# Performance work log

Measured on AMD Instinct MI355X. Metric: run time of the kernel, lower is better.

Reference implementation:

```python
import jax, jax.numpy as jnp
import numpy as np

B = 512          # batch_size
C = 4            # num_classes
N = 16384        # grid unknowns per sample (128x128)
H = 0.0078125    # grid spacing h = 1/128


def setup_inputs() -> dict:
    key = jax.random.key(0)
    k1, k2, k3 = jax.random.split(key, 3)
    coefficients = jax.random.uniform(k1, (B, N), dtype=jnp.float32)  # positive -> A SPD
    predictions = jax.random.normal(k2, (B, C, N), dtype=jnp.float32)
    targets = jax.random.normal(k3, (B, N, C), dtype=jnp.float32)
    return {"coefficients": coefficients, "predictions": predictions, "targets": targets}


def reference(coefficients, predictions, targets):
    # A = diag(h^2 * coefficients[i]); exploit diagonality: A @ v == a * v.
    a = (H * H) * coefficients                      # [B, N] diagonal of A per sample
    preds = predictions.reshape(B, C, -1)           # predictions.view(batch_size, num_classes, -1)

    # Modified Gram-Schmidt in the A-inner product, vectorized over batch.
    ortho = []
    for j in range(C):                              # tiny fixed loop over classes
        v = preds[:, j, :]                          # [B, N]
        for e in ortho:
            proj = jnp.sum(v * (a * e), axis=-1, keepdims=True)  # <v, A e>
            v = v - proj * e
        n2 = jnp.sum(v * a * v, axis=-1, keepdims=True)          # <v, A v>
        safe = jnp.where(n2 > 0, n2, jnp.float32(1.0))
        v = jnp.where(n2 > 0, v * jax.lax.rsqrt(safe), v)        # normalize iff <v,Av> > 0
        ortho.append(v)
    Cm = jnp.stack(ortho, axis=1)                   # [B, C, N]

    # M = C_i @ A @ targets[i] for each sample -> [B, C, C]
    M = jnp.einsum('bcn,bnm->bcm', Cm * a[:, None, :], targets)
    per_sample = (jnp.float32(4.0) - jnp.sum(M * M, axis=(1, 2))) / jnp.float32(4.0)
    return jnp.mean(per_sample)
```

## Files before the change

### kernel.cpp

```cpp
#include <hip/hip_runtime.h>

#define BSZ 512
#define NC  4
#define NN  16384
#define H2  (0.0078125f * 0.0078125f)

#define BLK   512
#define SPLIT 2
#define GROUPS_PER_BLOCK (NN / 4 / SPLIT)
#define ITERS (GROUPS_PER_BLOCK / BLK)

__device__ __forceinline__ void accum_elem(float a,
                                           float p0, float p1, float p2, float p3,
                                           float tx, float ty, float tz, float tw,
                                           float* acc)
{
    float ap0 = a * p0, ap1 = a * p1, ap2 = a * p2, ap3 = a * p3;
    acc[0]  += ap0 * p0;  acc[1]  += ap0 * p1;  acc[2]  += ap0 * p2;  acc[3]  += ap0 * p3;
    acc[4]  += ap1 * p1;  acc[5]  += ap1 * p2;  acc[6]  += ap1 * p3;
    acc[7]  += ap2 * p2;  acc[8]  += ap2 * p3;
    acc[9]  += ap3 * p3;
    acc[10] += ap0 * tx;  acc[11] += ap0 * ty;  acc[12] += ap0 * tz;  acc[13] += ap0 * tw;
    acc[14] += ap1 * tx;  acc[15] += ap1 * ty;  acc[16] += ap1 * tz;  acc[17] += ap1 * tw;
    acc[18] += ap2 * tx;  acc[19] += ap2 * ty;  acc[20] += ap2 * tz;  acc[21] += ap2 * tw;
    acc[22] += ap3 * tx;  acc[23] += ap3 * ty;  acc[24] += ap3 * tz;  acc[25] += ap3 * tw;
}

__global__ __launch_bounds__(BLK)
void loss_part(const float* __restrict__ coef,
               const float* __restrict__ pred,
               const float* __restrict__ targ,
               float* __restrict__ partial)
{
    const int blk = blockIdx.x;
    const int b   = blk / SPLIT;
    const int s   = blk % SPLIT;
    const int tid = threadIdx.x;

    const float4* __restrict__ c4 = (const float4*)(coef + (size_t)b * NN);
    const float4* __restrict__ q0 = (const float4*)(pred + (size_t)b * NC * NN + 0 * NN);
    const float4* __restrict__ q1 = (const float4*)(pred + (size_t)b * NC * NN + 1 * NN);
    const float4* __restrict__ q2 = (const float4*)(pred + (size_t)b * NC * NN + 2 * NN);
    const float4* __restrict__ q3 = (const float4*)(pred + (size_t)b * NC * NN + 3 * NN);
    const float4* __restrict__ t4 = (const float4*)(targ + (size_t)b * NN * NC);

    const int g0 = s * GROUPS_PER_BLOCK;

    float acc[26];
#pragma unroll
    for (int k = 0; k < 26; ++k) acc[k] = 0.f;

    for (int k = 0; k < ITERS; ++k) {
        const int i = g0 + k * BLK + tid;
        float4 cc = c4[i];
        float4 a0 = q0[i];
        float4 a1 = q1[i];
        float4 a2 = q2[i];
        float4 a3 = q3[i];
        float4 t0 = t4[4 * i + 0];
        float4 t1 = t4[4 * i + 1];
        float4 t2 = t4[4 * i + 2];
        float4 t3 = t4[4 * i + 3];

        accum_elem(H2 * cc.x, a0.x, a1.x, a2.x, a3.x, t0.x, t0.y, t0.z, t0.w, acc);
        accum_elem(H2 * cc.y, a0.y, a1.y, a2.y, a3.y, t1.x, t1.y, t1.z, t1.w, acc);
        accum_elem(H2 * cc.z, a0.z, a1.z, a2.z, a3.z, t2.x, t2.y, t2.z, t2.w, acc);
        accum_elem(H2 * cc.w, a0.w, a1.w, a2.w, a3.w, t3.x, t3.y, t3.z, t3.w, acc);
    }

    const int lane = tid & 63;
    const int wv   = tid >> 6;
    __shared__ float red[26][8];

#pragma unroll
    for (int k = 0; k < 26; ++k) {
        float v = acc[k];
#pragma unroll
        for (int o = 32; o > 0; o >>= 1) v += __shfl_down(v, o, 64);
        if (lane == 0) red[k][wv] = v;
    }
    __syncthreads();

    if (tid < 26) {
        float v = 0.f;
#pragma unroll
        for (int w = 0; w < 8; ++w) v += red[tid][w];
        partial[(size_t)blk * 26 + tid] = v;
    }
}

__global__ __launch_bounds__(BSZ)
void loss_final(const float* __restrict__ partial, float* __restrict__ out)
{
    const int b = threadIdx.x;

    float s[26];
#pragma unroll
    for (int k = 0; k < 26; ++k) {
        float v = 0.f;
#pragma unroll
        for (int p = 0; p < SPLIT; ++p)
            v += partial[(size_t)(b * SPLIT + p) * 26 + k];
        s[k] = v;
    }

    float Gm[4][4];
    Gm[0][0] = s[0];
    Gm[0][1] = Gm[1][0] = s[1];
    Gm[0][2] = Gm[2][0] = s[2];
    Gm[0][3] = Gm[3][0] = s[3];
    Gm[1][1] = s[4];
    Gm[1][2] = Gm[2][1] = s[5];
    Gm[1][3] = Gm[3][1] = s[6];
    Gm[2][2] = s[7];
    Gm[2][3] = Gm[3][2] = s[8];
    Gm[3][3] = s[9];

    float Tm[4][4];
#pragma unroll
    for (int i = 0; i < 4; ++i)
#pragma unroll
        for (int m = 0; m < 4; ++m) Tm[i][m] = s[10 + 4 * i + m];

    float u[4][4];
#pragma unroll
    for (int j = 0; j < 4; ++j) {
        float w[4];
#pragma unroll
        for (int i = 0; i < 4; ++i) w[i] = (i == j) ? 1.f : 0.f;
#pragma unroll
        for (int k = 0; k < 4; ++k) {
            if (k < j) {
                float proj = 0.f;
#pragma unroll
                for (int i = 0; i < 4; ++i) {
                    float gu = 0.f;
#pragma unroll
                    for (int l = 0; l < 4; ++l) gu += Gm[i][l] * u[k][l];
                    proj += w[i] * gu;
                }
#pragma unroll
                for (int i = 0; i < 4; ++i) w[i] -= proj * u[k][i];
            }
        }
        float n2 = 0.f;
#pragma unroll
        for (int i = 0; i < 4; ++i) {
            float gw = 0.f;
#pragma unroll
            for (int l = 0; l < 4; ++l) gw += Gm[i][l] * w[l];
            n2 += w[i] * gw;
        }
        float sc = (n2 > 0.f) ? rsqrtf(n2) : 1.f;
#pragma unroll
        for (int i = 0; i < 4; ++i) u[j][i] = w[i] * sc;
    }

    float ssum = 0.f;
#pragma unroll
    for (int c = 0; c < 4; ++c) {
#pragma unroll
        for (int m = 0; m < 4; ++m) {
            float M = 0.f;
#pragma unroll
            for (int i = 0; i < 4; ++i) M += u[c][i] * Tm[i][m];
            ssum += M * M;
        }
    }
    float ps = (4.f - ssum) * 0.25f;

    const int lane = b & 63;
    const int wv   = b >> 6;
#pragma unroll
    for (int o = 32; o > 0; o >>= 1) ps += __shfl_down(ps, o, 64);
    __shared__ float red[8];
    if (lane == 0) red[wv] = ps;
    __syncthreads();
    if (b == 0) {
        float tot = 0.f;
#pragma unroll
        for (int w = 0; w < 8; ++w) tot += red[w];
        out[0] = tot / (float)BSZ;
    }
}

extern "C" void kernel_launch(void* const* d_in, const int* in_sizes, int n_in,
                              void* d_out, int out_size, void* d_ws, size_t ws_size,
                              hipStream_t stream)
{
    const float* coef = (const float*)d_in[0];
    const float* pred = (const float*)d_in[1];
    const float* targ = (const float*)d_in[2];
    float* out = (float*)d_out;
    float* partial = (float*)d_ws;

    loss_part<<<BSZ * SPLIT, BLK, 0, stream>>>(coef, pred, targ, partial);
    loss_final<<<1, BSZ, 0, stream>>>(partial, out);
}
```

Before: 305.5 us.

## Switch to scalar per-element loads with software prefetch of next iteration

Each thread now handles one grid element per iteration, using scalar loads for coefficient and predictions and one float4 load for the target row, instead of float4 groups of four elements. The next iteration's data is loaded into registers before the current accumulation, a manual double-buffer meant to overlap memory latency with FMA work. This cuts loads in flight per thread from nine float4s to five scalar-or-float4 loads, which may lower achieved bandwidth, and the loop runs four times as many iterations.

```diff
diff --git a/kernel.cpp b/kernel.cpp
--- a/kernel.cpp
+++ b/kernel.cpp
@@ -7,24 +7,9 @@
 
 #define BLK   512
 #define SPLIT 2
-#define GROUPS_PER_BLOCK (NN / 4 / SPLIT)
-#define ITERS (GROUPS_PER_BLOCK / BLK)
+#define ELEMS_PER_BLOCK (NN / SPLIT)
+#define ITERS (ELEMS_PER_BLOCK / BLK)
 
-__device__ __forceinline__ void accum_elem(float a,
-                                           float p0, float p1, float p2, float p3,
-                                           float tx, float ty, float tz, float tw,
-                                           float* acc)
-{
-    float ap0 = a * p0, ap1 = a * p1, ap2 = a * p2, ap3 = a * p3;
-    acc[0]  += ap0 * p0;  acc[1]  += ap0 * p1;  acc[2]  += ap0 * p2;  acc[3]  += ap0 * p3;
-    acc[4]  += ap1 * p1;  acc[5]  += ap1 * p2;  acc[6]  += ap1 * p3;
-    acc[7]  += ap2 * p2;  acc[8]  += ap2 * p3;
-    acc[9]  += ap3 * p3;
-    acc[10] += ap0 * tx;  acc[11] += ap0 * ty;  acc[12] += ap0 * tz;  acc[13] += ap0 * tw;
-    acc[14] += ap1 * tx;  acc[15] += ap1 * ty;  acc[16] += ap1 * tz;  acc[17] += ap1 * tw;
-    acc[18] += ap2 * tx;  acc[19] += ap2 * ty;  acc[20] += ap2 * tz;  acc[21] += ap2 * tw;
-    acc[22] += ap3 * tx;  acc[23] += ap3 * ty;  acc[24] += ap3 * tz;  acc[25] += ap3 * tw;
-}
 
 __global__ __launch_bounds__(BLK)
 void loss_part(const float* __restrict__ coef,
@@ -37,35 +22,47 @@
     const int s   = blk % SPLIT;
     const int tid = threadIdx.x;
 
-    const float4* __restrict__ c4 = (const float4*)(coef + (size_t)b * NN);
-    const float4* __restrict__ q0 = (const float4*)(pred + (size_t)b * NC * NN + 0 * NN);
-    const float4* __restrict__ q1 = (const float4*)(pred + (size_t)b * NC * NN + 1 * NN);
-    const float4* __restrict__ q2 = (const float4*)(pred + (size_t)b * NC * NN + 2 * NN);
-    const float4* __restrict__ q3 = (const float4*)(pred + (size_t)b * NC * NN + 3 * NN);
+    const float* __restrict__ c  = coef + (size_t)b * NN;
+    const float* __restrict__ q0 = pred + (size_t)b * NC * NN + 0 * NN;
+    const float* __restrict__ q1 = pred + (size_t)b * NC * NN + 1 * NN;
+    const float* __restrict__ q2 = pred + (size_t)b * NC * NN + 2 * NN;
+    const float* __restrict__ q3 = pred + (size_t)b * NC * NN + 3 * NN;
     const float4* __restrict__ t4 = (const float4*)(targ + (size_t)b * NN * NC);
-
-    const int g0 = s * GROUPS_PER_BLOCK;
 
     float acc[26];
 #pragma unroll
     for (int k = 0; k < 26; ++k) acc[k] = 0.f;
 
+    int n = s * ELEMS_PER_BLOCK + tid;
+
+    float  cN  = c[n];
+    float  p0N = q0[n], p1N = q1[n], p2N = q2[n], p3N = q3[n];
+    float4 tN  = t4[n];
+
+#pragma unroll 1
     for (int k = 0; k < ITERS; ++k) {
-        const int i = g0 + k * BLK + tid;
-        float4 cc = c4[i];
-        float4 a0 = q0[i];
-        float4 a1 = q1[i];
-        float4 a2 = q2[i];
-        float4 a3 = q3[i];
-        float4 t0 = t4[4 * i + 0];
-        float4 t1 = t4[4 * i + 1];
-        float4 t2 = t4[4 * i + 2];
-        float4 t3 = t4[4 * i + 3];
+        const float  cc = cN;
+        const float  p0 = p0N, p1 = p1N, p2 = p2N, p3 = p3N;
+        const float4 tt = tN;
 
-        accum_elem(H2 * cc.x, a0.x, a1.x, a2.x, a3.x, t0.x, t0.y, t0.z, t0.w, acc);
-        accum_elem(H2 * cc.y, a0.y, a1.y, a2.y, a3.y, t1.x, t1.y, t1.z, t1.w, acc);
-        accum_elem(H2 * cc.z, a0.z, a1.z, a2.z, a3.z, t2.x, t2.y, t2.z, t2.w, acc);
-        accum_elem(H2 * cc.w, a0.w, a1.w, a2.w, a3.w, t3.x, t3.y, t3.z, t3.w, acc);
+        if (k + 1 < ITERS) {
+            const int n2 = n + BLK;
+            cN  = c[n2];
+            p0N = q0[n2]; p1N = q1[n2]; p2N = q2[n2]; p3N = q3[n2];
+            tN  = t4[n2];
+            n   = n2;
+        }
+
+        const float a   = H2 * cc;
+        const float ap0 = a * p0, ap1 = a * p1, ap2 = a * p2, ap3 = a * p3;
+        acc[0]  += ap0 * p0;  acc[1]  += ap0 * p1;  acc[2]  += ap0 * p2;  acc[3]  += ap0 * p3;
+        acc[4]  += ap1 * p1;  acc[5]  += ap1 * p2;  acc[6]  += ap1 * p3;
+        acc[7]  += ap2 * p2;  acc[8]  += ap2 * p3;
+        acc[9]  += ap3 * p3;
+        acc[10] += ap0 * tt.x;  acc[11] += ap0 * tt.y;  acc[12] += ap0 * tt.z;  acc[13] += ap0 * tt.w;
+        acc[14] += ap1 * tt.x;  acc[15] += ap1 * tt.y;  acc[16] += ap1 * tt.z;  acc[17] += ap1 * tt.w;
+        acc[18] += ap2 * tt.x;  acc[19] += ap2 * tt.y;  acc[20] += ap2 * tt.z;  acc[21] += ap2 * tt.w;
+        acc[22] += ap3 * tt.x;  acc[23] += ap3 * tt.y;  acc[24] += ap3 * tt.z;  acc[25] += ap3 * tt.w;
     }
 
     const int lane = tid & 63;
```

Result: no change. 305.9 us (+0.1%).
